# Kernel optimization log

Measured on AMD Instinct MI355X. Metric: run time of the kernel, lower is better.

## Reference

```python
import jax, jax.numpy as jnp
import numpy as np

N_NODES = 10000
N_EDGES = 640000
IN_FEATS = 128
OUT_FEATS = 512


def setup_inputs() -> dict:
    key = jax.random.key(0)
    k1, k2, k3, k4, k5 = jax.random.split(key, 5)
    x = jax.random.normal(k1, (N_NODES, IN_FEATS), dtype=jnp.float32)
    src = jax.random.randint(k2, (N_EDGES,), 0, N_NODES, dtype=jnp.int32)
    dst = jax.random.randint(k3, (N_EDGES,), 0, N_NODES, dtype=jnp.int32)
    W = jax.random.normal(k4, (IN_FEATS, OUT_FEATS), dtype=jnp.float32) / np.sqrt(IN_FEATS)
    b = jax.random.normal(k5, (OUT_FEATS,), dtype=jnp.float32) * 0.01
    return {"x": x, "src": src, "dst": dst, "W": W, "b": b}


def reference(x, src, dst, W, b):
    # gather source features per edge: [E, F]
    msgs = x[src]
    # segment-sum into destination nodes, plus in-degree for the mean
    sums = jax.ops.segment_sum(msgs, dst, num_segments=N_NODES)  # [N, F]
    deg = jax.ops.segment_sum(jnp.ones((N_EDGES,), dtype=x.dtype), dst, num_segments=N_NODES)  # [N]
    mean = sums / jnp.maximum(deg, 1.0)[:, None]
    # DGL recv only updates nodes that received messages; zero-in-degree nodes keep inputs
    h = jnp.where(deg[:, None] > 0, mean, x)
    # linear projection
    return h @ W + b
```

## Files before the change

### kernel.cpp

```cpp
#include <hip/hip_runtime.h>

#define IN_F 128
#define OUT_F 512
#define NPB 20
#define NBKT 500
#define BCAP 1664
#define STRIPE 4096
#define LCAP 24
#define MAXDEG 128

typedef float f32x4 __attribute__((ext_vector_type(4)));
typedef __bf16 bf16x8 __attribute__((ext_vector_type(8)));

static __device__ __forceinline__ unsigned short bf16_rne(float f) {
    unsigned u = __float_as_uint(f);
    return (unsigned short)((u + 0x7FFFu + ((u >> 16) & 1u)) >> 16);
}

__global__ __launch_bounds__(256) void pack_kernel(
    const float* __restrict__ x, unsigned int* __restrict__ xh,
    const float* __restrict__ W, unsigned short* __restrict__ wt,
    int* __restrict__ bcnt, int total2, int xblocks) {
    int blk = blockIdx.x;
    if (blk == 0) {
        for (int i = threadIdx.x; i < NBKT; i += 256) bcnt[i] = 0;
    }
    if (blk < xblocks) {
        int i = blk * 256 + threadIdx.x;
        if (i < total2) {
            float2 v = *reinterpret_cast<const float2*>(&x[i * 2]);
            unsigned int ux = (unsigned int)bf16_rne(v.x);
            unsigned int uy = (unsigned int)bf16_rne(v.y);
            xh[i] = ux | (uy << 16);
        }
    } else {
        int wblk = blk - xblocks;
#pragma unroll
        for (int rep = 0; rep < 2; ++rep) {
            int idx = wblk * 512 + rep * 256 + threadIdx.x;
            int n = idx & (OUT_F - 1);
            int k = idx >> 9;
            wt[n * IN_F + k] = bf16_rne(W[idx]);
        }
    }
}

__global__ __launch_bounds__(1024) void fill_kernel(
    const int* __restrict__ src, const int* __restrict__ dst,
    unsigned int* __restrict__ bins,
    int* __restrict__ bcnt, int E) {
    __shared__ unsigned int lbin[NBKT][LCAP];
    __shared__ int lcnt[NBKT];
    __shared__ int lbase[NBKT];
    const int t = threadIdx.x;
    for (int i = t; i < NBKT; i += 1024) lcnt[i] = 0;
    __syncthreads();

    const int e0 = blockIdx.x * STRIPE;
    for (int i = t; i < STRIPE; i += 1024) {
        int e = e0 + i;
        if (e < E) {
            int d = dst[e];
            int s = src[e];
            int b = d / NPB;
            int dl = d - b * NPB;
            unsigned int ent = (unsigned)s | ((unsigned)dl << 16);
            int p = atomicAdd(&lcnt[b], 1);
            if (p < LCAP) {
                lbin[b][p] = ent;
            } else {
                int g = atomicAdd(&bcnt[b], 1);
                if (g < BCAP) bins[b * BCAP + g] = ent;
            }
        }
    }
    __syncthreads();

    for (int i = t; i < NBKT; i += 1024) {
        int c = min(lcnt[i], LCAP);
        lcnt[i] = c;
        lbase[i] = atomicAdd(&bcnt[i], c);
    }
    __syncthreads();

    const int lane = t & 63, w = t >> 6;
    for (int b = w; b < NBKT; b += 16) {
        int c = lcnt[b];
        int gb = lbase[b];
        if (lane < c) {
            int gp = gb + lane;
            if (gp < BCAP) bins[b * BCAP + gp] = lbin[b][lane];
        }
    }
}

__global__ __launch_bounds__(1024, 8) void mega_kernel(
    const unsigned int* __restrict__ xh, const unsigned int* __restrict__ bins,
    const int* __restrict__ bcnt, const unsigned short* __restrict__ wt,
    const float* __restrict__ bias, float* __restrict__ out, int N) {
    __shared__ unsigned short ssrc[NPB][MAXDEG];
    __shared__ int cur[NPB];
    __shared__ unsigned int hsm[32][68];
    const int b = blockIdx.x, t = threadIdx.x;
    const int cnt = min(bcnt[b], BCAP);
    const unsigned int* bp = bins + (size_t)b * BCAP;

    if (t < NPB) cur[t] = 0;
    __syncthreads();

    for (int i = t; i < cnt; i += 1024) {
        unsigned int ent = bp[i];
        int dl = (int)(ent >> 16);
        int p = atomicAdd(&cur[dl], 1);
        if (p < MAXDEG) ssrc[dl][p] = (unsigned short)(ent & 0xFFFFu);
    }
    __syncthreads();

    const int lane = t & 63, w = t >> 6;
    const int sub = lane >> 4, l16 = lane & 15;

#define ACCUM(P)                                   \
    acc[0] += __uint_as_float((P).x << 16);        \
    acc[1] += __uint_as_float((P).x & 0xFFFF0000u);\
    acc[2] += __uint_as_float((P).y << 16);        \
    acc[3] += __uint_as_float((P).y & 0xFFFF0000u);\
    acc[4] += __uint_as_float((P).z << 16);        \
    acc[5] += __uint_as_float((P).z & 0xFFFF0000u);\
    acc[6] += __uint_as_float((P).w << 16);        \
    acc[7] += __uint_as_float((P).w & 0xFFFF0000u);

    for (int dl = w; dl < NPB; dl += 16) {
        const int dcnt = cur[dl];
        const int m = min(dcnt, MAXDEG);
        float acc[8];
#pragma unroll
        for (int k = 0; k < 8; ++k) acc[k] = 0.f;
        int i = sub;
        for (; i + 12 < m; i += 16) {
            int s0 = (int)ssrc[dl][i];
            int s1 = (int)ssrc[dl][i + 4];
            int s2 = (int)ssrc[dl][i + 8];
            int s3 = (int)ssrc[dl][i + 12];
            uint4 p0 = *reinterpret_cast<const uint4*>(&xh[s0 * (IN_F / 2) + l16 * 4]);
            uint4 p1 = *reinterpret_cast<const uint4*>(&xh[s1 * (IN_F / 2) + l16 * 4]);
            uint4 p2 = *reinterpret_cast<const uint4*>(&xh[s2 * (IN_F / 2) + l16 * 4]);
            uint4 p3 = *reinterpret_cast<const uint4*>(&xh[s3 * (IN_F / 2) + l16 * 4]);
            ACCUM(p0) ACCUM(p1) ACCUM(p2) ACCUM(p3)
        }
        for (; i < m; i += 4) {
            int s = (int)ssrc[dl][i];
            uint4 p = *reinterpret_cast<const uint4*>(&xh[s * (IN_F / 2) + l16 * 4]);
            ACCUM(p)
        }
#pragma unroll
        for (int k = 0; k < 8; ++k) {
            acc[k] += __shfl_xor(acc[k], 16);
            acc[k] += __shfl_xor(acc[k], 32);
        }
        if (sub == 0) {
            const int node = b * NPB + dl;
            if (dcnt > 0) {
                float inv = 1.f / (float)dcnt;
#pragma unroll
                for (int j = 0; j < 4; ++j) {
                    unsigned lo = bf16_rne(acc[2 * j] * inv);
                    unsigned hi = bf16_rne(acc[2 * j + 1] * inv);
                    hsm[dl][l16 * 4 + j] = lo | (hi << 16);
                }
            } else {
                uint4 v = *reinterpret_cast<const uint4*>(&xh[node * (IN_F / 2) + l16 * 4]);
                hsm[dl][l16 * 4 + 0] = v.x;
                hsm[dl][l16 * 4 + 1] = v.y;
                hsm[dl][l16 * 4 + 2] = v.z;
                hsm[dl][l16 * 4 + 3] = v.w;
            }
        }
    }
#undef ACCUM
    __syncthreads();

    const int lq = lane >> 4;
    const int wn = w * 32;
    f32x4 acc2[2][2];
#pragma unroll
    for (int mt = 0; mt < 2; ++mt)
#pragma unroll
        for (int nt = 0; nt < 2; ++nt) acc2[mt][nt] = {0.f, 0.f, 0.f, 0.f};

#pragma unroll
    for (int kk = 0; kk < 4; ++kk) {
        const int kb = kk * 32 + lq * 8;
        const int kb2 = kk * 16 + lq * 4;
        bf16x8 a8[2];
#pragma unroll
        for (int mt = 0; mt < 2; ++mt) {
            uint4 av = *reinterpret_cast<const uint4*>(&hsm[mt * 16 + l16][kb2]);
            a8[mt] = __builtin_bit_cast(bf16x8, av);
        }
#pragma unroll
        for (int nt = 0; nt < 2; ++nt) {
            const int gc = wn + nt * 16 + l16;
            bf16x8 bh = *reinterpret_cast<const bf16x8*>(&wt[gc * IN_F + kb]);
#pragma unroll
            for (int mt = 0; mt < 2; ++mt) {
                acc2[mt][nt] = __builtin_amdgcn_mfma_f32_16x16x32_bf16(
                    a8[mt], bh, acc2[mt][nt], 0, 0, 0);
            }
        }
    }

#pragma unroll
    for (int nt = 0; nt < 2; ++nt) {
        const int gc = wn + nt * 16 + l16;
        const float bv = bias[gc];
#pragma unroll
        for (int mt = 0; mt < 2; ++mt) {
            const int rloc = mt * 16 + lq * 4;
#pragma unroll
            for (int j = 0; j < 4; ++j) {
                int rr = rloc + j;
                if (rr < NPB)
                    out[(size_t)(b * NPB + rr) * OUT_F + gc] = acc2[mt][nt][j] + bv;
            }
        }
    }
}

extern "C" void kernel_launch(void* const* d_in, const int* in_sizes, int n_in,
                              void* d_out, int out_size, void* d_ws, size_t ws_size,
                              hipStream_t stream) {
    const float* x   = (const float*)d_in[0];
    const int*   src = (const int*)d_in[1];
    const int*   dst = (const int*)d_in[2];
    const float* W   = (const float*)d_in[3];
    const float* b   = (const float*)d_in[4];
    float*       out = (float*)d_out;

    const int N = in_sizes[0] / IN_F;
    const int E = in_sizes[1];

    char* ws = (char*)d_ws;
    unsigned int* bins = (unsigned int*)ws;
    int* bcnt = (int*)((char*)bins + (size_t)NBKT * BCAP * 4);
    unsigned int* xh = (unsigned int*)(bcnt + NBKT + 12);
    unsigned short* wt = (unsigned short*)(xh + N * IN_F / 2);

    int total2 = N * IN_F / 2;
    int xblocks = (total2 + 255) / 256;
    int wblocks = (IN_F * OUT_F) / 512;
    pack_kernel<<<xblocks + wblocks, 256, 0, stream>>>(x, xh, W, wt, bcnt,
                                                       total2, xblocks);

    int fb = (E + STRIPE - 1) / STRIPE;
    fill_kernel<<<fb, 1024, 0, stream>>>(src, dst, bins, bcnt, E);

    mega_kernel<<<NBKT, 1024, 0, stream>>>(xh, bins, bcnt, wt, b, out, N);
}
```

Measured before the change: 42.80 us.

## Merge pack and fill into one prep kernel with atomic-free per-stripe bin segments

Merges the bf16 packing of x and W and the edge bucketing into a single launch. Each fill block now writes its edges into a fixed per-(bucket, stripe) slot range with a count array, instead of reserving space through global atomics with an overflow path. Buckets grow to 32 nodes, so the 32-row MFMA tile is fully used and there are fewer blocks. The cost is that any stripe giving a bucket more than 48 edges silently drops them, and the gather kernel must scan every padded slot and check it against the per-stripe counts.

```diff
diff --git a/kernel.cpp b/kernel.cpp
--- a/kernel.cpp
+++ b/kernel.cpp
@@ -2,11 +2,12 @@
 
 #define IN_F 128
 #define OUT_F 512
-#define NPB 20
-#define NBKT 500
-#define BCAP 1664
+#define NPB 32
+#define NBKT 313
 #define STRIPE 4096
-#define LCAP 24
+#define FB 157
+#define LCAP 48
+#define SEGTOT (FB * LCAP)
 #define MAXDEG 128
 
 typedef float f32x4 __attribute__((ext_vector_type(4)));
@@ -17,16 +18,43 @@
     return (unsigned short)((u + 0x7FFFu + ((u >> 16) & 1u)) >> 16);
 }
 
-__global__ __launch_bounds__(256) void pack_kernel(
+#define XPB 625
+#define WPB 64
+__global__ __launch_bounds__(1024) void prep_kernel(
     const float* __restrict__ x, unsigned int* __restrict__ xh,
     const float* __restrict__ W, unsigned short* __restrict__ wt,
-    int* __restrict__ bcnt, int total2, int xblocks) {
-    int blk = blockIdx.x;
-    if (blk == 0) {
-        for (int i = threadIdx.x; i < NBKT; i += 256) bcnt[i] = 0;
-    }
-    if (blk < xblocks) {
-        int i = blk * 256 + threadIdx.x;
+    const int* __restrict__ src, const int* __restrict__ dst,
+    unsigned int* __restrict__ bins, int* __restrict__ bseg,
+    int E, int total2) {
+    __shared__ unsigned int lbin[NBKT][LCAP];
+    __shared__ int lcnt[NBKT];
+    const int blk = blockIdx.x;
+    const int t = threadIdx.x;
+
+    if (blk < FB) {
+        for (int i = t; i < NBKT; i += 1024) lcnt[i] = 0;
+        __syncthreads();
+        const int e0 = blk * STRIPE;
+        for (int i = t; i < STRIPE; i += 1024) {
+            int e = e0 + i;
+            if (e < E) {
+                int d = dst[e];
+                int s = src[e];
+                int b = d >> 5, dl = d & 31;
+                int p = atomicAdd(&lcnt[b], 1);
+                if (p < LCAP) lbin[b][p] = (unsigned)s | ((unsigned)dl << 16);
+            }
+        }
+        __syncthreads();
+        const int lane = t & 63, w = t >> 6;
+        for (int b = w; b < NBKT; b += 16) {
+            int c = min(lcnt[b], LCAP);
+            if (lane < c)
+                bins[(size_t)b * SEGTOT + blk * LCAP + lane] = lbin[b][lane];
+            if (lane == 0) bseg[b * FB + blk] = c;
+        }
+    } else if (blk < FB + XPB) {
+        int i = (blk - FB) * 1024 + t;
         if (i < total2) {
             float2 v = *reinterpret_cast<const float2*>(&x[i * 2]);
             unsigned int ux = (unsigned int)bf16_rne(v.x);
@@ -34,85 +62,37 @@
             xh[i] = ux | (uy << 16);
         }
     } else {
-        int wblk = blk - xblocks;
-#pragma unroll
-        for (int rep = 0; rep < 2; ++rep) {
-            int idx = wblk * 512 + rep * 256 + threadIdx.x;
-            int n = idx & (OUT_F - 1);
-            int k = idx >> 9;
-            wt[n * IN_F + k] = bf16_rne(W[idx]);
-        }
-    }
-}
-
-__global__ __launch_bounds__(1024) void fill_kernel(
-    const int* __restrict__ src, const int* __restrict__ dst,
-    unsigned int* __restrict__ bins,
-    int* __restrict__ bcnt, int E) {
-    __shared__ unsigned int lbin[NBKT][LCAP];
-    __shared__ int lcnt[NBKT];
-    __shared__ int lbase[NBKT];
-    const int t = threadIdx.x;
-    for (int i = t; i < NBKT; i += 1024) lcnt[i] = 0;
-    __syncthreads();
-
-    const int e0 = blockIdx.x * STRIPE;
-    for (int i = t; i < STRIPE; i += 1024) {
-        int e = e0 + i;
-        if (e < E) {
-            int d = dst[e];
-            int s = src[e];
-            int b = d / NPB;
-            int dl = d - b * NPB;
-            unsigned int ent = (unsigned)s | ((unsigned)dl << 16);
-            int p = atomicAdd(&lcnt[b], 1);
-            if (p < LCAP) {
-                lbin[b][p] = ent;
-            } else {
-                int g = atomicAdd(&bcnt[b], 1);
-                if (g < BCAP) bins[b * BCAP + g] = ent;
-            }
-        }
-    }
-    __syncthreads();
-
-    for (int i = t; i < NBKT; i += 1024) {
-        int c = min(lcnt[i], LCAP);
-        lcnt[i] = c;
-        lbase[i] = atomicAdd(&bcnt[i], c);
-    }
-    __syncthreads();
-
-    const int lane = t & 63, w = t >> 6;
-    for (int b = w; b < NBKT; b += 16) {
-        int c = lcnt[b];
-        int gb = lbase[b];
-        if (lane < c) {
-            int gp = gb + lane;
-            if (gp < BCAP) bins[b * BCAP + gp] = lbin[b][lane];
-        }
+        int idx = (blk - FB - XPB) * 1024 + t;
+        int n = idx & (OUT_F - 1);
+        int k = idx >> 9;
+        wt[n * IN_F + k] = bf16_rne(W[idx]);
     }
 }
 
 __global__ __launch_bounds__(1024, 8) void mega_kernel(
     const unsigned int* __restrict__ xh, const unsigned int* __restrict__ bins,
-    const int* __restrict__ bcnt, const unsigned short* __restrict__ wt,
+    const int* __restrict__ bseg, const unsigned short* __restrict__ wt,
     const float* __restrict__ bias, float* __restrict__ out, int N) {
     __shared__ unsigned short ssrc[NPB][MAXDEG];
     __shared__ int cur[NPB];
+    __shared__ int scnt[FB];
     __shared__ unsigned int hsm[32][68];
     const int b = blockIdx.x, t = threadIdx.x;
-    const int cnt = min(bcnt[b], BCAP);
-    const unsigned int* bp = bins + (size_t)b * BCAP;
-
+    const unsigned int* bp = bins + (size_t)b * SEGTOT;
+
+    for (int i = t; i < FB; i += 1024) scnt[i] = bseg[b * FB + i];
     if (t < NPB) cur[t] = 0;
     __syncthreads();
 
-    for (int i = t; i < cnt; i += 1024) {
-        unsigned int ent = bp[i];
-        int dl = (int)(ent >> 16);
-        int p = atomicAdd(&cur[dl], 1);
-        if (p < MAXDEG) ssrc[dl][p] = (unsigned short)(ent & 0xFFFFu);
+    for (int slot = t; slot < SEGTOT; slot += 1024) {
+        int i = slot / LCAP;
+        int j = slot - i * LCAP;
+        if (j < scnt[i]) {
+            unsigned int ent = bp[slot];
+            int dl = (int)(ent >> 16);
+            int p = atomicAdd(&cur[dl], 1);
+            if (p < MAXDEG) ssrc[dl][p] = (unsigned short)(ent & 0xFFFFu);
+        }
     }
     __syncthreads();
 
@@ -130,6 +110,8 @@
     acc[7] += __uint_as_float((P).w & 0xFFFF0000u);
 
     for (int dl = w; dl < NPB; dl += 16) {
+        const int node = b * NPB + dl;
+        if (node >= N) continue;
         const int dcnt = cur[dl];
         const int m = min(dcnt, MAXDEG);
         float acc[8];
@@ -158,7 +140,6 @@
             acc[k] += __shfl_xor(acc[k], 32);
         }
         if (sub == 0) {
-            const int node = b * NPB + dl;
             if (dcnt > 0) {
                 float inv = 1.f / (float)dcnt;
 #pragma unroll
@@ -218,9 +199,9 @@
             const int rloc = mt * 16 + lq * 4;
 #pragma unroll
             for (int j = 0; j < 4; ++j) {
-                int rr = rloc + j;
-                if (rr < NPB)
-                    out[(size_t)(b * NPB + rr) * OUT_F + gc] = acc2[mt][nt][j] + bv;
+                int node = b * NPB + rloc + j;
+                if (node < N)
+                    out[(size_t)node * OUT_F + gc] = acc2[mt][nt][j] + bv;
             }
         }
     }
@@ -241,18 +222,12 @@
 
     char* ws = (char*)d_ws;
     unsigned int* bins = (unsigned int*)ws;
-    int* bcnt = (int*)((char*)bins + (size_t)NBKT * BCAP * 4);
-    unsigned int* xh = (unsigned int*)(bcnt + NBKT + 12);
-    unsigned short* wt = (unsigned short*)(xh + N * IN_F / 2);
+    int* bseg = (int*)((char*)bins + (size_t)NBKT * SEGTOT * 4);
+    unsigned int* xh = (unsigned int*)(bseg + NBKT * FB);
+    unsigned short* wt = (unsigned short*)(xh + (size_t)N * IN_F / 2);
 
     int total2 = N * IN_F / 2;
-    int xblocks = (total2 + 255) / 256;
-    int wblocks = (IN_F * OUT_F) / 512;
-    pack_kernel<<<xblocks + wblocks, 256, 0, stream>>>(x, xh, W, wt, bcnt,
-                                                       total2, xblocks);
-
-    int fb = (E + STRIPE - 1) / STRIPE;
-    fill_kernel<<<fb, 1024, 0, stream>>>(src, dst, bins, bcnt, E);
-
-    mega_kernel<<<NBKT, 1024, 0, stream>>>(xh, bins, bcnt, wt, b, out, N);
-}
+    prep_kernel<<<FB + XPB + WPB, 1024, 0, stream>>>(x, xh, W, wt, src, dst,
+                                                     bins, bseg, E, total2);
+    mega_kernel<<<NBKT, 1024, 0, stream>>>(xh, bins, bseg, wt, b, out, N);
+}
```

Measured after the change: 45.87 us. +7.2%, slower.

## Use 16-node buckets with 512-thread blocks to remove padded MFMA rows

Applied to the files above, without the earlier changes.

Bucket width drops from 20 to 16 nodes, so the final bf16 MFMA projection uses one 16-row tile per block instead of two tiles that were partly padding. Blocks shrink to 512 threads (8 waves, each covering 64 output columns), and the grid grows to 625 buckets. Bucket indexing becomes shift and mask instead of division, and the per-bucket capacity shrinks to match. The trade-off is more blocks, a higher chance of bucket overflow with the smaller capacity, and fewer waves sharing the gather work in each block.

```diff
diff --git a/kernel.cpp b/kernel.cpp
--- a/kernel.cpp
+++ b/kernel.cpp
@@ -2,9 +2,9 @@
 
 #define IN_F 128
 #define OUT_F 512
-#define NPB 20
-#define NBKT 500
-#define BCAP 1664
+#define NPB 16
+#define NBKT 625
+#define BCAP 1344
 #define STRIPE 4096
 #define LCAP 24
 #define MAXDEG 128
@@ -22,8 +22,9 @@
     const float* __restrict__ W, unsigned short* __restrict__ wt,
     int* __restrict__ bcnt, int total2, int xblocks) {
     int blk = blockIdx.x;
-    if (blk == 0) {
-        for (int i = threadIdx.x; i < NBKT; i += 256) bcnt[i] = 0;
+    if (blk < 3) {
+        int i = blk * 256 + threadIdx.x;
+        if (i < NBKT) bcnt[i] = 0;
     }
     if (blk < xblocks) {
         int i = blk * 256 + threadIdx.x;
@@ -62,15 +63,14 @@
         if (e < E) {
             int d = dst[e];
             int s = src[e];
-            int b = d / NPB;
-            int dl = d - b * NPB;
+            int b = d >> 4, dl = d & 15;
             unsigned int ent = (unsigned)s | ((unsigned)dl << 16);
             int p = atomicAdd(&lcnt[b], 1);
             if (p < LCAP) {
                 lbin[b][p] = ent;
             } else {
                 int g = atomicAdd(&bcnt[b], 1);
-                if (g < BCAP) bins[b * BCAP + g] = ent;
+                if (g < BCAP) bins[(size_t)b * BCAP + g] = ent;
             }
         }
     }
@@ -89,18 +89,18 @@
         int gb = lbase[b];
         if (lane < c) {
             int gp = gb + lane;
-            if (gp < BCAP) bins[b * BCAP + gp] = lbin[b][lane];
-        }
-    }
-}
-
-__global__ __launch_bounds__(1024, 8) void mega_kernel(
+            if (gp < BCAP) bins[(size_t)b * BCAP + gp] = lbin[b][lane];
+        }
+    }
+}
+
+__global__ __launch_bounds__(512, 4) void mega_kernel(
     const unsigned int* __restrict__ xh, const unsigned int* __restrict__ bins,
     const int* __restrict__ bcnt, const unsigned short* __restrict__ wt,
     const float* __restrict__ bias, float* __restrict__ out, int N) {
     __shared__ unsigned short ssrc[NPB][MAXDEG];
     __shared__ int cur[NPB];
-    __shared__ unsigned int hsm[32][68];
+    __shared__ unsigned int hsm[NPB][68];
     const int b = blockIdx.x, t = threadIdx.x;
     const int cnt = min(bcnt[b], BCAP);
     const unsigned int* bp = bins + (size_t)b * BCAP;
@@ -108,7 +108,7 @@
     if (t < NPB) cur[t] = 0;
     __syncthreads();
 
-    for (int i = t; i < cnt; i += 1024) {
+    for (int i = t; i < cnt; i += 512) {
         unsigned int ent = bp[i];
         int dl = (int)(ent >> 16);
         int p = atomicAdd(&cur[dl], 1);
@@ -129,7 +129,8 @@
     acc[6] += __uint_as_float((P).w << 16);        \
     acc[7] += __uint_as_float((P).w & 0xFFFF0000u);
 
-    for (int dl = w; dl < NPB; dl += 16) {
+    for (int dl = w; dl < NPB; dl += 8) {
+        const int node = b * NPB + dl;
         const int dcnt = cur[dl];
         const int m = min(dcnt, MAXDEG);
         float acc[8];
@@ -158,7 +159,6 @@
             acc[k] += __shfl_xor(acc[k], 32);
         }
         if (sub == 0) {
-            const int node = b * NPB + dl;
             if (dcnt > 0) {
                 float inv = 1.f / (float)dcnt;
 #pragma unroll
@@ -180,48 +180,34 @@
     __syncthreads();
 
     const int lq = lane >> 4;
-    const int wn = w * 32;
-    f32x4 acc2[2][2];
-#pragma unroll
-    for (int mt = 0; mt < 2; ++mt)
-#pragma unroll
-        for (int nt = 0; nt < 2; ++nt) acc2[mt][nt] = {0.f, 0.f, 0.f, 0.f};
+    const int wn = w * 64;
+    f32x4 acc2[4];
+#pragma unroll
+    for (int nt = 0; nt < 4; ++nt) acc2[nt] = {0.f, 0.f, 0.f, 0.f};
 
 #pragma unroll
     for (int kk = 0; kk < 4; ++kk) {
         const int kb = kk * 32 + lq * 8;
         const int kb2 = kk * 16 + lq * 4;
-        bf16x8 a8[2];
-#pragma unroll
-        for (int mt = 0; mt < 2; ++mt) {
-            uint4 av = *reinterpret_cast<const uint4*>(&hsm[mt * 16 + l16][kb2]);
-            a8[mt] = __builtin_bit_cast(bf16x8, av);
-        }
-#pragma unroll
-        for (int nt = 0; nt < 2; ++nt) {
+        uint4 av = *reinterpret_cast<const uint4*>(&hsm[l16][kb2]);
+        bf16x8 a8 = __builtin_bit_cast(bf16x8, av);
+#pragma unroll
+        for (int nt = 0; nt < 4; ++nt) {
             const int gc = wn + nt * 16 + l16;
             bf16x8 bh = *reinterpret_cast<const bf16x8*>(&wt[gc * IN_F + kb]);
-#pragma unroll
-            for (int mt = 0; mt < 2; ++mt) {
-                acc2[mt][nt] = __builtin_amdgcn_mfma_f32_16x16x32_bf16(
-                    a8[mt], bh, acc2[mt][nt], 0, 0, 0);
-            }
-        }
-    }
-
-#pragma unroll
-    for (int nt = 0; nt < 2; ++nt) {
+            acc2[nt] = __builtin_amdgcn_mfma_f32_16x16x32_bf16(a8, bh, acc2[nt], 0, 0, 0);
+        }
+    }
+
+#pragma unroll
+    for (int nt = 0; nt < 4; ++nt) {
         const int gc = wn + nt * 16 + l16;
         const float bv = bias[gc];
 #pragma unroll
-        for (int mt = 0; mt < 2; ++mt) {
-            const int rloc = mt * 16 + lq * 4;
-#pragma unroll
-            for (int j = 0; j < 4; ++j) {
-                int rr = rloc + j;
-                if (rr < NPB)
-                    out[(size_t)(b * NPB + rr) * OUT_F + gc] = acc2[mt][nt][j] + bv;
-            }
+        for (int j = 0; j < 4; ++j) {
+            int node = b * NPB + lq * 4 + j;
+            if (node < N)
+                out[(size_t)node * OUT_F + gc] = acc2[nt][j] + bv;
         }
     }
 }
@@ -242,8 +228,8 @@
     char* ws = (char*)d_ws;
     unsigned int* bins = (unsigned int*)ws;
     int* bcnt = (int*)((char*)bins + (size_t)NBKT * BCAP * 4);
-    unsigned int* xh = (unsigned int*)(bcnt + NBKT + 12);
-    unsigned short* wt = (unsigned short*)(xh + N * IN_F / 2);
+    unsigned int* xh = (unsigned int*)(bcnt + NBKT + 15);
+    unsigned short* wt = (unsigned short*)(xh + (size_t)N * IN_F / 2);
 
     int total2 = N * IN_F / 2;
     int xblocks = (total2 + 255) / 256;
@@ -254,5 +240,5 @@
     int fb = (E + STRIPE - 1) / STRIPE;
     fill_kernel<<<fb, 1024, 0, stream>>>(src, dst, bins, bcnt, E);
 
-    mega_kernel<<<NBKT, 1024, 0, stream>>>(xh, bins, bcnt, wt, b, out, N);
-}
+    mega_kernel<<<NBKT, 512, 0, stream>>>(xh, bins, bcnt, wt, b, out, N);
+}
```

New measurement: 51.30 us (median of 2 runs). 1.2x slower.
